# Kernel tuning notes

Hardware: AMD Instinct MI355X
Metric: run time of the kernel (lower is better)

## Reference

```python
import jax, jax.numpy as jnp
import numpy as np

B, S, IN_DIM, OUT_DIM, G = 8, 2048, 512, 256, 8
CHUNK = 128  # positions per scan step; per-chunk phi = CHUNK*O*O*G floats
EPS = 1e-5   # torch LayerNorm default


def make_periods():
    # periods[i,j,g] = i*(O*G) + j*G + g + 2
    i = jnp.arange(OUT_DIM, dtype=jnp.float32)[:, None, None]
    j = jnp.arange(OUT_DIM, dtype=jnp.float32)[None, :, None]
    g = jnp.arange(G, dtype=jnp.float32)[None, None, :]
    return i * (OUT_DIM * G) + j * G + g + 2.0


def setup_inputs() -> dict:
    key = jax.random.key(0)
    ks = jax.random.split(key, 4)
    x = jax.random.normal(ks[0], (B, S, IN_DIM), dtype=jnp.float32)
    positions = jnp.arange(S, dtype=jnp.int64 if jax.config.jax_enable_x64 else jnp.int32)
    M = jax.random.uniform(ks[1], (OUT_DIM, IN_DIM), minval=-0.5, maxval=0.5, dtype=jnp.float32)
    P = jax.random.uniform(ks[2], (OUT_DIM, OUT_DIM, G), minval=-0.1, maxval=0.1, dtype=jnp.float32)
    W_res = jax.random.uniform(ks[3], (OUT_DIM, IN_DIM), minval=-0.1, maxval=0.1, dtype=jnp.float32)
    ln_scale = jnp.ones((OUT_DIM,), dtype=jnp.float32)
    ln_bias = jnp.zeros((OUT_DIM,), dtype=jnp.float32)
    periods = make_periods()
    return {"x": x, "M": M, "P": P, "W_res": W_res, "ln_scale": ln_scale,
            "ln_bias": ln_bias, "periods": periods, "positions": positions}


def layer_norm(h, scale, bias):
    mu = jnp.mean(h, axis=-1, keepdims=True)
    var = jnp.mean(jnp.square(h - mu), axis=-1, keepdims=True)  # biased, like torch
    return (h - mu) * jax.lax.rsqrt(var + EPS) * scale + bias


def reference(x, M, P, W_res, ln_scale, ln_bias, periods, positions):
    # x: (B,S,in), M: (out,in), P: (out,out,G), periods: (out,out,G)
    x_trans = layer_norm(jnp.einsum('bsi,oi->bso', x, M), ln_scale, ln_bias)

    two_pi = jnp.float32(2.0 * np.pi)
    pos_chunks = positions.astype(jnp.float32).reshape(-1, CHUNK)  # (S/CHUNK, CHUNK)

    def body(carry, pos):
        # phi: (CHUNK, O, O, G); reduce over g first to avoid the huge 5D tensor
        phi = jnp.cos(two_pi * pos[:, None, None, None] / periods)
        A = jnp.einsum('sijg,ijg->sij', phi, P)  # (CHUNK, O, O)
        return carry, A

    _, A = jax.lax.scan(body, 0, pos_chunks)
    A = A.reshape(S, OUT_DIM, OUT_DIM)  # A[s,i,j] = sum_g P[i,j,g]*cos(2*pi*k_s/T_ijg)

    Nk = jnp.einsum('bsj,sij->bsi', x_trans, A)  # (B,S,out)
    residual = jnp.einsum('bsi,oi->bso', x, W_res)  # separate residual proj
    return Nk + residual
```

## Files before the change

kernel.cpp:

```cpp
#include <hip/hip_runtime.h>
#include <hip/hip_bf16.h>
#include <math.h>

#define B_   8
#define S_   2048
#define IN_  512
#define OUT_ 256
#define G_   8


typedef float  f32x2  __attribute__((ext_vector_type(2)));
typedef float  f32x4  __attribute__((ext_vector_type(4)));
typedef short  s16x8  __attribute__((ext_vector_type(8)));
typedef __bf16 bf16x8 __attribute__((ext_vector_type(8)));
typedef unsigned short u16x8 __attribute__((ext_vector_type(8)));

__device__ __forceinline__ float cos2pi(float f) {
#if __has_builtin(__builtin_amdgcn_cosf)
    return __builtin_amdgcn_cosf(f);
#else
    return __cosf(6.28318530717958647692f * f);
#endif
}

__device__ __forceinline__ float fractf_(float f) {
#if __has_builtin(__builtin_amdgcn_fractf)
    return __builtin_amdgcn_fractf(f);
#else
    return f - floorf(f);
#endif
}

__device__ __forceinline__ unsigned short f2bf(float f) {
    unsigned u = __builtin_bit_cast(unsigned, f);
    u += 0x7fffu + ((u >> 16) & 1u);
    return (unsigned short)(u >> 16);
}

template <typename T>
__device__ __forceinline__ auto atomF_(T* p, T v, int) -> decltype(unsafeAtomicAdd(p, v)) {
    return unsafeAtomicAdd(p, v);
}
template <typename T>
__device__ __forceinline__ T atomF_(T* p, T v, long) {
    return atomicAdd(p, v);
}
__device__ __forceinline__ void atomAddF(float* p, float v) { atomF_(p, v, 0); }

template <typename T>
__device__ __forceinline__ auto mfma_bf16_(T a, T b, f32x4 c, int)
    -> decltype(__builtin_amdgcn_mfma_f32_16x16x32_bf16(a, b, c, 0, 0, 0)) {
    return __builtin_amdgcn_mfma_f32_16x16x32_bf16(a, b, c, 0, 0, 0);
}
template <typename T>
__device__ __forceinline__ auto mfma_bf16_(T a, T b, f32x4 c, long)
    -> decltype(__builtin_amdgcn_mfma_f32_16x16x32_bf16(__builtin_bit_cast(bf16x8, a),
                                                        __builtin_bit_cast(bf16x8, b), c, 0, 0, 0)) {
    return __builtin_amdgcn_mfma_f32_16x16x32_bf16(__builtin_bit_cast(bf16x8, a),
                                                   __builtin_bit_cast(bf16x8, b), c, 0, 0, 0);
}
__device__ __forceinline__ f32x4 mfma_bf16(s16x8 a, s16x8 b, f32x4 c) {
    return mfma_bf16_(a, b, c, 0);
}

__device__ __forceinline__ void gld16(const void* g, void* l) {
    __builtin_amdgcn_global_load_lds((const __attribute__((address_space(1))) unsigned int*)g,
                                     (__attribute__((address_space(3))) unsigned int*)l,
                                     16, 0, 0);
}

__device__ __forceinline__ f32x2 lo2(float4 v) { f32x2 r; r.x = v.x; r.y = v.y; return r; }
__device__ __forceinline__ f32x2 hi2(float4 v) { f32x2 r; r.x = v.z; r.y = v.w; return r; }

__device__ __forceinline__ void prep_one(const float* __restrict__ P,
                                         const float* __restrict__ periods,
                                         float4* __restrict__ PTK, int tid) {
    const int j = tid >> 8, i = tid & 255;
    float p[8], iT[8], k2[8];
#pragma unroll
    for (int g = 0; g < 8; ++g) {
        const int idx = (i * 256 + j) * 8 + g;
        p[g]  = P[idx];
        iT[g] = 1.0f / periods[idx];
        k2[g] = 2.0f * cos2pi(iT[g]);
    }
    float4* base = PTK + (size_t)(j * 6) * 256 + i;
    base[0]    = make_float4(p[0],  p[1],  p[2],  p[3]);
    base[256]  = make_float4(p[4],  p[5],  p[6],  p[7]);
    base[512]  = make_float4(iT[0], iT[1], iT[2], iT[3]);
    base[768]  = make_float4(iT[4], iT[5], iT[6], iT[7]);
    base[1024] = make_float4(k2[0], k2[1], k2[2], k2[3]);
    base[1280] = make_float4(k2[4], k2[5], k2[6], k2[7]);
}

__global__ __launch_bounds__(256) void cvt_prep(const float* __restrict__ x,
                                                const float* __restrict__ M,
                                                const float* __restrict__ Wres,
                                                const float* __restrict__ P,
                                                const float* __restrict__ periods,
                                                unsigned short* __restrict__ Xb,
                                                unsigned short* __restrict__ Wb,
                                                float4* __restrict__ PTK) {
    const int bid = blockIdx.x;
    if (bid >= 4224) {
        prep_one(P, periods, PTK, (bid - 4224) * 256 + threadIdx.x);
        return;
    }
    const float* src;
    unsigned short* dst;
    if (bid < 4096) {
        const int idx = bid * 256 + threadIdx.x;
        src = x + (size_t)idx * 8;
        dst = Xb + (size_t)idx * 8;
    } else {
        const int idx = (bid - 4096) * 256 + threadIdx.x;
        const int row = idx >> 6;
        const int col = (idx & 63) * 8;
        src = (row < 256) ? (M + (size_t)row * 512 + col)
                          : (Wres + (size_t)(row - 256) * 512 + col);
        dst = Wb + (size_t)row * 512 + col;
    }
    const float4 v0 = *(const float4*)(src);
    const float4 v1 = *(const float4*)(src + 4);
    u16x8 o;
    o[0] = f2bf(v0.x); o[1] = f2bf(v0.y); o[2] = f2bf(v0.z); o[3] = f2bf(v0.w);
    o[4] = f2bf(v1.x); o[5] = f2bf(v1.y); o[6] = f2bf(v1.z); o[7] = f2bf(v1.w);
    *(u16x8*)dst = o;
}

__global__ __launch_bounds__(256) void cvt_xw(const float* __restrict__ x,
                                              const float* __restrict__ M,
                                              const float* __restrict__ Wres,
                                              unsigned short* __restrict__ Xb,
                                              unsigned short* __restrict__ Wb) {
    const int bid = blockIdx.x;
    const float* src;
    unsigned short* dst;
    if (bid < 4096) {
        const int idx = bid * 256 + threadIdx.x;
        src = x + (size_t)idx * 8;
        dst = Xb + (size_t)idx * 8;
    } else {
        const int idx = (bid - 4096) * 256 + threadIdx.x;
        const int row = idx >> 6;
        const int col = (idx & 63) * 8;
        src = (row < 256) ? (M + (size_t)row * 512 + col)
                          : (Wres + (size_t)(row - 256) * 512 + col);
        dst = Wb + (size_t)row * 512 + col;
    }
    const float4 v0 = *(const float4*)(src);
    const float4 v1 = *(const float4*)(src + 4);
    u16x8 o;
    o[0] = f2bf(v0.x); o[1] = f2bf(v0.y); o[2] = f2bf(v0.z); o[3] = f2bf(v0.w);
    o[4] = f2bf(v1.x); o[5] = f2bf(v1.y); o[6] = f2bf(v1.z); o[7] = f2bf(v1.w);
    *(u16x8*)dst = o;
}

__global__ __launch_bounds__(256) void prep_ptk(const float* __restrict__ P,
                                                const float* __restrict__ periods,
                                                float4* __restrict__ PTK) {
    prep_one(P, periods, PTK, blockIdx.x * 256 + threadIdx.x);
}

__global__ __launch_bounds__(256) void gemm_mfma(const unsigned short* __restrict__ Xb,
                                                 const unsigned short* __restrict__ Wb,
                                                 float* __restrict__ y,
                                                 float* __restrict__ out) {
    __shared__ __align__(16) unsigned short At[64 * 64];
    __shared__ __align__(16) unsigned short Bt[128 * 64];
    const int t    = threadIdx.x;
    const int col0 = blockIdx.x * 128;
    const int row0 = blockIdx.y * 64;

    const unsigned short* ga[2]; int la[2];
    const unsigned short* gb[4]; int lb[4];
#pragma unroll
    for (int cc = 0; cc < 2; ++cc) {
        const int L = cc * 256 + t;
        const int r = L >> 3;
        const int c = (L & 7) ^ (r & 7);
        ga[cc] = Xb + (size_t)(row0 + r) * 512 + c * 8;
        la[cc] = L * 8;
    }
#pragma unroll
    for (int cc = 0; cc < 4; ++cc) {
        const int L = cc * 256 + t;
        const int r = L >> 3;
        const int c = (L & 7) ^ (r & 7);
        gb[cc] = Wb + (size_t)(col0 + r) * 512 + c * 8;
        lb[cc] = L * 8;
    }

    const int lane = t & 63;
    const int wave = t >> 6;
    const int wn   = wave * 32;
    const int quad = lane >> 4;
    const int l16  = lane & 15;

    f32x4 acc[4][2];
#pragma unroll
    for (int mi = 0; mi < 4; ++mi)
#pragma unroll
        for (int ni = 0; ni < 2; ++ni) acc[mi][ni] = {0.0f, 0.0f, 0.0f, 0.0f};

    for (int k0 = 0; k0 < 512; k0 += 64) {
        __syncthreads();
#pragma unroll
        for (int cc = 0; cc < 2; ++cc) gld16(ga[cc] + k0, At + la[cc]);
#pragma unroll
        for (int cc = 0; cc < 4; ++cc) gld16(gb[cc] + k0, Bt + lb[cc]);
        __syncthreads();
#pragma unroll
        for (int ks = 0; ks < 2; ++ks) {
            const int cc = (ks * 4 + quad) ^ (l16 & 7);
            s16x8 af[4], bf[2];
#pragma unroll
            for (int mi = 0; mi < 4; ++mi) {
                const int ra = mi * 16 + l16;
                af[mi] = *(const s16x8*)(At + (ra * 8 + cc) * 8);
            }
#pragma unroll
            for (int ni = 0; ni < 2; ++ni) {
                const int rb = wn + ni * 16 + l16;
                bf[ni] = *(const s16x8*)(Bt + (rb * 8 + cc) * 8);
            }
#pragma unroll
            for (int mi = 0; mi < 4; ++mi)
#pragma unroll
                for (int ni = 0; ni < 2; ++ni)
                    acc[mi][ni] = mfma_bf16(af[mi], bf[ni], acc[mi][ni]);
        }
    }

    float* dst   = (col0 < 256) ? y : out;
    const int cb = (col0 & 255) + wn;
#pragma unroll
    for (int mi = 0; mi < 4; ++mi) {
        const int rbase = row0 + mi * 16 + quad * 4;
#pragma unroll
        for (int ni = 0; ni < 2; ++ni) {
            const int col = cb + ni * 16 + l16;
#pragma unroll
            for (int rg = 0; rg < 4; ++rg)
                dst[(size_t)(rbase + rg) * 256 + col] = acc[mi][ni][rg];
        }
    }
}

__global__ __launch_bounds__(256) void gemm_kernel(const float* __restrict__ x,
                                                   const float* __restrict__ M,
                                                   const float* __restrict__ Wres,
                                                   float* __restrict__ y,
                                                   float* __restrict__ out) {
    __shared__ float As[8][132];
    __shared__ float Bs[8][132];
    const int ct = blockIdx.x;
    const int rt = blockIdx.y;
    const int t  = threadIdx.x;
    const int row0 = rt * 128;
    const float* W = (ct < 2) ? M : Wres;
    const int wcol0 = (ct & 1) * 128;
    float acc[8][8];
#pragma unroll
    for (int r = 0; r < 8; ++r)
#pragma unroll
        for (int c = 0; c < 8; ++c) acc[r][c] = 0.0f;
    const int lr = t >> 1;
    const int lk = (t & 1) << 2;
    for (int k0 = 0; k0 < 512; k0 += 8) {
        float4 av = *(const float4*)(x + (size_t)(row0 + lr) * 512 + k0 + lk);
        float4 bv = *(const float4*)(W + (size_t)(wcol0 + lr) * 512 + k0 + lk);
        __syncthreads();
        As[lk + 0][lr] = av.x; As[lk + 1][lr] = av.y; As[lk + 2][lr] = av.z; As[lk + 3][lr] = av.w;
        Bs[lk + 0][lr] = bv.x; Bs[lk + 1][lr] = bv.y; Bs[lk + 2][lr] = bv.z; Bs[lk + 3][lr] = bv.w;
        __syncthreads();
        const int tx = t & 15, ty = t >> 4;
#pragma unroll
        for (int kk = 0; kk < 8; ++kk) {
            const float4 a0 = *(const float4*)&As[kk][ty * 8];
            const float4 a1 = *(const float4*)&As[kk][ty * 8 + 4];
            const float4 b0 = *(const float4*)&Bs[kk][tx * 8];
            const float4 b1 = *(const float4*)&Bs[kk][tx * 8 + 4];
            const float ar[8] = {a0.x, a0.y, a0.z, a0.w, a1.x, a1.y, a1.z, a1.w};
            const float br[8] = {b0.x, b0.y, b0.z, b0.w, b1.x, b1.y, b1.z, b1.w};
#pragma unroll
            for (int r = 0; r < 8; ++r)
#pragma unroll
                for (int c = 0; c < 8; ++c) acc[r][c] = fmaf(ar[r], br[c], acc[r][c]);
        }
    }
    const int tx = t & 15, ty = t >> 4;
    float* dst = (ct < 2) ? y : out;
    const int cbase = (ct & 1) * 128 + tx * 8;
#pragma unroll
    for (int r = 0; r < 8; ++r) {
        float4 v0 = {acc[r][0], acc[r][1], acc[r][2], acc[r][3]};
        float4 v1 = {acc[r][4], acc[r][5], acc[r][6], acc[r][7]};
        float* p = dst + (size_t)(row0 + ty * 8 + r) * 256 + cbase;
        *(float4*)(p)     = v0;
        *(float4*)(p + 4) = v1;
    }
}

__global__ __launch_bounds__(256) void ln_kernel(float* __restrict__ y,
                                                 const float* __restrict__ scale,
                                                 const float* __restrict__ bias) {
    const int t    = threadIdx.x;
    const int row  = blockIdx.x * 4 + (t >> 6);
    const int lane = t & 63;
    float* p = y + (size_t)row * 256 + lane * 4;
    float4 v = *(float4*)p;
    float s  = v.x + v.y + v.z + v.w;
    float ss = v.x * v.x + v.y * v.y + v.z * v.z + v.w * v.w;
#pragma unroll
    for (int off = 32; off > 0; off >>= 1) {
        s  += __shfl_xor(s, off);
        ss += __shfl_xor(ss, off);
    }
    const float mu  = s * (1.0f / 256.0f);
    const float var = ss * (1.0f / 256.0f) - mu * mu;
    const float rs  = rsqrtf(var + 1e-5f);
    float4 sc = *(const float4*)(scale + lane * 4);
    float4 bi = *(const float4*)(bias + lane * 4);
    float4 o;
    o.x = (v.x - mu) * rs * sc.x + bi.x;
    o.y = (v.y - mu) * rs * sc.y + bi.y;
    o.z = (v.z - mu) * rs * sc.z + bi.z;
    o.w = (v.w - mu) * rs * sc.w + bi.w;
    *(float4*)p = o;
}

__global__ __launch_bounds__(256, 4) void cosnk_pk(const float4* __restrict__ PTK,
                                                   const float* __restrict__ xt,
                                                   float* __restrict__ out) {
    __shared__ float xs[128 * 64];
    const int t  = threadIdx.x;
    const int bx = blockIdx.x;
    const int ih = (bx >> 2) & 1;
    const int rid = ((bx >> 3) << 2) | (bx & 3);
    const int stile = rid >> 1;
    const int jh = rid & 1;
    const int s0 = stile * 8;
    const int jbase = jh * 128;

    {
        const int slot = t >> 2;
        const int st   = slot >> 3;
        const int b    = slot & 7;
        const int jg   = t & 3;
        const float* src = xt + (size_t)(b * S_ + s0 + st) * 256 + jbase + jg * 32;
#pragma unroll
        for (int q = 0; q < 8; ++q) {
            float4 v = *(const float4*)(src + 4 * q);
            const int jl = jg * 32 + 4 * q;
            xs[(jl + 0) * 64 + slot] = v.x;
            xs[(jl + 1) * 64 + slot] = v.y;
            xs[(jl + 2) * 64 + slot] = v.z;
            xs[(jl + 3) * 64 + slot] = v.w;
        }
    }
    __syncthreads();

    const int i   = ih * 128 + (t & 127);
    const int jq  = t >> 7;
    const int jl0 = jq * 64;
    const float sv0 = (float)s0;
    f32x2 sv0v; sv0v.x = sv0; sv0v.y = sv0;

    f32x2 accP[8][4];
#pragma unroll
    for (int s = 0; s < 8; ++s)
#pragma unroll
        for (int q = 0; q < 4; ++q) { accP[s][q].x = 0.0f; accP[s][q].y = 0.0f; }

    const float4* ptk = PTK + (size_t)(jbase + jl0) * 1536 + i;
    float4 qp0 = ptk[0],    qp1 = ptk[256];
    float4 qt0 = ptk[512],  qt1 = ptk[768];
    float4 qk0 = ptk[1024], qk1 = ptk[1280];

#define CHEBP(p2_, t2_, k2_)                                \
    do {                                                    \
        f32x2 f0 = sv0v * (t2_);                            \
        f0.x = fractf_(f0.x); f0.y = fractf_(f0.y);         \
        f32x2 c0; c0.x = cos2pi(f0.x); c0.y = cos2pi(f0.y); \
        f32x2 f1 = f0 + (t2_);                              \
        f1.x = fractf_(f1.x); f1.y = fractf_(f1.y);         \
        f32x2 c1; c1.x = cos2pi(f1.x); c1.y = cos2pi(f1.y); \
        f32x2 c2 = (k2_) * c1 - c0;                         \
        f32x2 c3 = (k2_) * c2 - c1;                         \
        f32x2 c4 = (k2_) * c3 - c2;                         \
        f32x2 c5 = (k2_) * c4 - c3;                         \
        f32x2 c6 = (k2_) * c5 - c4;                         \
        f32x2 c7 = (k2_) * c6 - c5;                         \
        A0 += (p2_) * c0; A1 += (p2_) * c1;                 \
        A2 += (p2_) * c2; A3 += (p2_) * c3;                 \
        A4 += (p2_) * c4; A5 += (p2_) * c5;                 \
        A6 += (p2_) * c6; A7 += (p2_) * c7;                 \
    } while (0)

    for (int jj = 0; jj < 64; ++jj) {
        const float4* pn = ptk + ((jj < 63) ? 1536 : 0);
        const float4 n0 = pn[0],   n1 = pn[256],  n2 = pn[512];
        const float4 n3 = pn[768], n4 = pn[1024], n5 = pn[1280];

        f32x2 A0 = {0.f, 0.f}, A1 = {0.f, 0.f}, A2 = {0.f, 0.f}, A3 = {0.f, 0.f};
        f32x2 A4 = {0.f, 0.f}, A5 = {0.f, 0.f}, A6 = {0.f, 0.f}, A7 = {0.f, 0.f};
        CHEBP(lo2(qp0), lo2(qt0), lo2(qk0));
        CHEBP(hi2(qp0), hi2(qt0), hi2(qk0));
        CHEBP(lo2(qp1), lo2(qt1), lo2(qk1));
        CHEBP(hi2(qp1), hi2(qt1), hi2(qk1));

        const float as_[8] = {A0.x + A0.y, A1.x + A1.y, A2.x + A2.y, A3.x + A3.y,
                              A4.x + A4.y, A5.x + A5.y, A6.x + A6.y, A7.x + A7.y};

        const float* xrow = &xs[(jl0 + jj) * 64];
#pragma unroll
        for (int s = 0; s < 8; ++s) {
            const float4 xa = *(const float4*)(xrow + s * 8);
            const float4 xb = *(const float4*)(xrow + s * 8 + 4);
            f32x2 av; av.x = as_[s]; av.y = as_[s];
            accP[s][0] += av * lo2(xa);
            accP[s][1] += av * hi2(xa);
            accP[s][2] += av * lo2(xb);
            accP[s][3] += av * hi2(xb);
        }
        qp0 = n0; qp1 = n1; qt0 = n2; qt1 = n3; qk0 = n4; qk1 = n5;
        ptk = pn;
    }
#undef CHEBP

    __syncthreads();
    const int tl = t & 127;
    if (jq) {
#pragma unroll
        for (int slot = 0; slot < 64; ++slot) {
            const int st = slot >> 3, b = slot & 7;
            xs[slot * 128 + tl] = accP[st][b >> 1][b & 1];
        }
    }
    __syncthreads();
    if (!jq) {
#pragma unroll
        for (int slot = 0; slot < 64; ++slot) {
            const int st = slot >> 3, b = slot & 7;
            const float v = accP[st][b >> 1][b & 1] + xs[slot * 128 + tl];
            atomAddF(&out[(size_t)(b * S_ + s0 + st) * 256 + i], v);
        }
    }
}

extern "C" void kernel_launch(void* const* d_in, const int* in_sizes, int n_in,
                              void* d_out, int out_size, void* d_ws, size_t ws_size,
                              hipStream_t stream) {
    const float* x        = (const float*)d_in[0];
    const float* M        = (const float*)d_in[1];
    const float* P        = (const float*)d_in[2];
    const float* Wres     = (const float*)d_in[3];
    const float* ln_scale = (const float*)d_in[4];
    const float* ln_bias  = (const float*)d_in[5];
    const float* periods  = (const float*)d_in[6];

    float* out = (float*)d_out;
    char*  wsb = (char*)d_ws;
    const size_t MB = 1024 * 1024;
    float* y = (float*)wsb;
    unsigned short* Xb = (unsigned short*)(wsb + 16 * MB);
    unsigned short* Wb = (unsigned short*)(wsb + 32 * MB);

    const bool big  = (ws_size >= 39 * MB);
    const bool mfma = (ws_size >= (size_t)34078720);

    float4* PTK;
    if (big) {
        PTK = (float4*)(wsb + 33 * MB);
        cvt_prep<<<4480, 256, 0, stream>>>(x, M, Wres, P, periods, Xb, Wb, PTK);
        dim3 ggrid(4, 256);
        gemm_mfma<<<ggrid, 256, 0, stream>>>(Xb, Wb, y, out);
    } else if (mfma) {
        PTK = (float4*)(wsb + 16 * MB);
        cvt_xw<<<4224, 256, 0, stream>>>(x, M, Wres, Xb, Wb);
        dim3 ggrid(4, 256);
        gemm_mfma<<<ggrid, 256, 0, stream>>>(Xb, Wb, y, out);
        prep_ptk<<<256, 256, 0, stream>>>(P, periods, PTK);
    } else {
        PTK = (float4*)(wsb + 16 * MB);
        dim3 ggrid(4, 128);
        gemm_kernel<<<ggrid, 256, 0, stream>>>(x, M, Wres, y, out);
        prep_ptk<<<256, 256, 0, stream>>>(P, periods, PTK);
    }

    ln_kernel<<<4096, 256, 0, stream>>>(y, ln_scale, ln_bias);

    cosnk_pk<<<1024, 256, 0, stream>>>(PTK, y, out);
}
```

Measured before the change: 234.4 us.

## Use fp16 dot2 for cos-weighted accumulation and shrink GEMM column tiles

```diff
diff --git a/kernel.cpp b/kernel.cpp
--- a/kernel.cpp
+++ b/kernel.cpp
@@ -9,11 +9,13 @@
 #define G_   8
 
 
-typedef float  f32x2  __attribute__((ext_vector_type(2)));
-typedef float  f32x4  __attribute__((ext_vector_type(4)));
-typedef short  s16x8  __attribute__((ext_vector_type(8)));
-typedef __bf16 bf16x8 __attribute__((ext_vector_type(8)));
+typedef float    f32x2  __attribute__((ext_vector_type(2)));
+typedef float    f32x4  __attribute__((ext_vector_type(4)));
+typedef short    s16x8  __attribute__((ext_vector_type(8)));
+typedef __bf16   bf16x8 __attribute__((ext_vector_type(8)));
 typedef unsigned short u16x8 __attribute__((ext_vector_type(8)));
+typedef _Float16 h2     __attribute__((ext_vector_type(2)));
+typedef _Float16 h16x8  __attribute__((ext_vector_type(8)));
 
 __device__ __forceinline__ float cos2pi(float f) {
 #if __has_builtin(__builtin_amdgcn_cosf)
@@ -36,6 +38,37 @@
     u += 0x7fffu + ((u >> 16) & 1u);
     return (unsigned short)(u >> 16);
 }
+
+__device__ __forceinline__ h2 pkrtz2(float a, float b) {
+#if __has_builtin(__builtin_amdgcn_cvt_pkrtz)
+    return __builtin_bit_cast(h2, __builtin_amdgcn_cvt_pkrtz(a, b));
+#else
+    h2 r; r[0] = (_Float16)a; r[1] = (_Float16)b; return r;
+#endif
+}
+
+#if __has_builtin(__builtin_amdgcn_fdot2)
+template <typename T>
+__device__ __forceinline__ auto fdot2_impl(T a, T b, float c, int)
+    -> decltype(__builtin_amdgcn_fdot2(a, b, c, false)) {
+    return __builtin_amdgcn_fdot2(a, b, c, false);
+}
+typedef __fp16 fp16v2 __attribute__((ext_vector_type(2)));
+template <typename T>
+__device__ __forceinline__ auto fdot2_impl(T a, T b, float c, long)
+    -> decltype(__builtin_amdgcn_fdot2(__builtin_bit_cast(fp16v2, a),
+                                       __builtin_bit_cast(fp16v2, b), c, false)) {
+    return __builtin_amdgcn_fdot2(__builtin_bit_cast(fp16v2, a),
+                                  __builtin_bit_cast(fp16v2, b), c, false);
+}
+__device__ __forceinline__ float fdot2_(h2 a, h2 b, float c) {
+    return fdot2_impl(a, b, c, 0);
+}
+#else
+__device__ __forceinline__ float fdot2_(h2 a, h2 b, float c) {
+    return c + (float)a[0] * (float)b[0] + (float)a[1] * (float)b[1];
+}
+#endif
 
 template <typename T>
 __device__ __forceinline__ auto atomF_(T* p, T v, int) -> decltype(unsafeAtomicAdd(p, v)) {
@@ -167,68 +200,58 @@
                                                  float* __restrict__ y,
                                                  float* __restrict__ out) {
     __shared__ __align__(16) unsigned short At[64 * 64];
-    __shared__ __align__(16) unsigned short Bt[128 * 64];
+    __shared__ __align__(16) unsigned short Bt[64 * 64];
     const int t    = threadIdx.x;
-    const int col0 = blockIdx.x * 128;
+    const int col0 = blockIdx.x * 64;
     const int row0 = blockIdx.y * 64;
 
     const unsigned short* ga[2]; int la[2];
-    const unsigned short* gb[4]; int lb[4];
+    const unsigned short* gb[2]; int lb[2];
 #pragma unroll
     for (int cc = 0; cc < 2; ++cc) {
         const int L = cc * 256 + t;
         const int r = L >> 3;
         const int c = (L & 7) ^ (r & 7);
         ga[cc] = Xb + (size_t)(row0 + r) * 512 + c * 8;
+        gb[cc] = Wb + (size_t)(col0 + r) * 512 + c * 8;
         la[cc] = L * 8;
-    }
-#pragma unroll
-    for (int cc = 0; cc < 4; ++cc) {
-        const int L = cc * 256 + t;
-        const int r = L >> 3;
-        const int c = (L & 7) ^ (r & 7);
-        gb[cc] = Wb + (size_t)(col0 + r) * 512 + c * 8;
         lb[cc] = L * 8;
     }
 
     const int lane = t & 63;
     const int wave = t >> 6;
-    const int wn   = wave * 32;
+    const int wn   = wave * 16;
     const int quad = lane >> 4;
     const int l16  = lane & 15;
 
-    f32x4 acc[4][2];
-#pragma unroll
-    for (int mi = 0; mi < 4; ++mi)
-#pragma unroll
-        for (int ni = 0; ni < 2; ++ni) acc[mi][ni] = {0.0f, 0.0f, 0.0f, 0.0f};
+    f32x4 acc[4];
+#pragma unroll
+    for (int mi = 0; mi < 4; ++mi) acc[mi] = {0.0f, 0.0f, 0.0f, 0.0f};
 
     for (int k0 = 0; k0 < 512; k0 += 64) {
         __syncthreads();
 #pragma unroll
-        for (int cc = 0; cc < 2; ++cc) gld16(ga[cc] + k0, At + la[cc]);
-#pragma unroll
-        for (int cc = 0; cc < 4; ++cc) gld16(gb[cc] + k0, Bt + lb[cc]);
+        for (int cc = 0; cc < 2; ++cc) {
+            gld16(ga[cc] + k0, At + la[cc]);
+            gld16(gb[cc] + k0, Bt + lb[cc]);
+        }
         __syncthreads();
 #pragma unroll
         for (int ks = 0; ks < 2; ++ks) {
             const int cc = (ks * 4 + quad) ^ (l16 & 7);
-            s16x8 af[4], bf[2];
+            s16x8 af[4], bf;
 #pragma unroll
             for (int mi = 0; mi < 4; ++mi) {
                 const int ra = mi * 16 + l16;
                 af[mi] = *(const s16x8*)(At + (ra * 8 + cc) * 8);
             }
-#pragma unroll
-            for (int ni = 0; ni < 2; ++ni) {
-                const int rb = wn + ni * 16 + l16;
-                bf[ni] = *(const s16x8*)(Bt + (rb * 8 + cc) * 8);
+            {
+                const int rb = wn + l16;
+                bf = *(const s16x8*)(Bt + (rb * 8 + cc) * 8);
             }
 #pragma unroll
             for (int mi = 0; mi < 4; ++mi)
-#pragma unroll
-                for (int ni = 0; ni < 2; ++ni)
-                    acc[mi][ni] = mfma_bf16(af[mi], bf[ni], acc[mi][ni]);
+                acc[mi] = mfma_bf16(af[mi], bf, acc[mi]);
         }
     }
 
@@ -237,13 +260,10 @@
 #pragma unroll
     for (int mi = 0; mi < 4; ++mi) {
         const int rbase = row0 + mi * 16 + quad * 4;
-#pragma unroll
-        for (int ni = 0; ni < 2; ++ni) {
-            const int col = cb + ni * 16 + l16;
-#pragma unroll
-            for (int rg = 0; rg < 4; ++rg)
-                dst[(size_t)(rbase + rg) * 256 + col] = acc[mi][ni][rg];
-        }
+        const int col = cb + l16;
+#pragma unroll
+        for (int rg = 0; rg < 4; ++rg)
+            dst[(size_t)(rbase + rg) * 256 + col] = acc[mi][rg];
     }
 }
 
@@ -330,10 +350,13 @@
     *(float4*)p = o;
 }
 
-__global__ __launch_bounds__(256, 4) void cosnk_pk(const float4* __restrict__ PTK,
+__global__ __launch_bounds__(256, 4) void cosnk_fd(const float4* __restrict__ PTK,
                                                    const float* __restrict__ xt,
                                                    float* __restrict__ out) {
-    __shared__ float xs[128 * 64];
+    __shared__ __align__(16) char smem[32768];
+    h2*    xsh = (h2*)smem;
+    float* red = (float*)smem;
+
     const int t  = threadIdx.x;
     const int bx = blockIdx.x;
     const int ih = (bx >> 2) & 1;
@@ -352,11 +375,9 @@
 #pragma unroll
         for (int q = 0; q < 8; ++q) {
             float4 v = *(const float4*)(src + 4 * q);
-            const int jl = jg * 32 + 4 * q;
-            xs[(jl + 0) * 64 + slot] = v.x;
-            xs[(jl + 1) * 64 + slot] = v.y;
-            xs[(jl + 2) * 64 + slot] = v.z;
-            xs[(jl + 3) * 64 + slot] = v.w;
+            const int jp = jg * 16 + 2 * q;
+            xsh[(jp + 0) * 64 + slot] = pkrtz2(v.x, v.y);
+            xsh[(jp + 1) * 64 + slot] = pkrtz2(v.z, v.w);
         }
     }
     __syncthreads();
@@ -367,16 +388,18 @@
     const float sv0 = (float)s0;
     f32x2 sv0v; sv0v.x = sv0; sv0v.y = sv0;
 
-    f32x2 accP[8][4];
+    float acc[8][8];
 #pragma unroll
     for (int s = 0; s < 8; ++s)
 #pragma unroll
-        for (int q = 0; q < 4; ++q) { accP[s][q].x = 0.0f; accP[s][q].y = 0.0f; }
+        for (int b = 0; b < 8; ++b) acc[s][b] = 0.0f;
 
     const float4* ptk = PTK + (size_t)(jbase + jl0) * 1536 + i;
     float4 qp0 = ptk[0],    qp1 = ptk[256];
     float4 qt0 = ptk[512],  qt1 = ptk[768];
     float4 qk0 = ptk[1024], qk1 = ptk[1280];
+
+    float asv[8];
 
 #define CHEBP(p2_, t2_, k2_)                                \
     do {                                                    \
@@ -398,6 +421,7 @@
         A6 += (p2_) * c6; A7 += (p2_) * c7;                 \
     } while (0)
 
+#pragma unroll 2
     for (int jj = 0; jj < 64; ++jj) {
         const float4* pn = ptk + ((jj < 63) ? 1536 : 0);
         const float4 n0 = pn[0],   n1 = pn[256],  n2 = pn[512];
@@ -413,16 +437,25 @@
         const float as_[8] = {A0.x + A0.y, A1.x + A1.y, A2.x + A2.y, A3.x + A3.y,
                               A4.x + A4.y, A5.x + A5.y, A6.x + A6.y, A7.x + A7.y};
 
-        const float* xrow = &xs[(jl0 + jj) * 64];
-#pragma unroll
-        for (int s = 0; s < 8; ++s) {
-            const float4 xa = *(const float4*)(xrow + s * 8);
-            const float4 xb = *(const float4*)(xrow + s * 8 + 4);
-            f32x2 av; av.x = as_[s]; av.y = as_[s];
-            accP[s][0] += av * lo2(xa);
-            accP[s][1] += av * hi2(xa);
-            accP[s][2] += av * lo2(xb);
-            accP[s][3] += av * hi2(xb);
+        if ((jj & 1) == 0) {
+#pragma unroll
+            for (int s = 0; s < 8; ++s) asv[s] = as_[s];
+        } else {
+            const h2* xrow = xsh + (size_t)(jq * 32 + (jj >> 1)) * 64;
+#pragma unroll
+            for (int s = 0; s < 8; ++s) {
+                const h2 ap = pkrtz2(asv[s], as_[s]);
+                const h16x8 hx0 = *(const h16x8*)(xrow + s * 8);
+                const h16x8 hx1 = *(const h16x8*)(xrow + s * 8 + 4);
+                acc[s][0] = fdot2_(ap, __builtin_shufflevector(hx0, hx0, 0, 1), acc[s][0]);
+                acc[s][1] = fdot2_(ap, __builtin_shufflevector(hx0, hx0, 2, 3), acc[s][1]);
+                acc[s][2] = fdot2_(ap, __builtin_shufflevector(hx0, hx0, 4, 5), acc[s][2]);
+                acc[s][3] = fdot2_(ap, __builtin_shufflevector(hx0, hx0, 6, 7), acc[s][3]);
+                acc[s][4] = fdot2_(ap, __builtin_shufflevector(hx1, hx1, 0, 1), acc[s][4]);
+                acc[s][5] = fdot2_(ap, __builtin_shufflevector(hx1, hx1, 2, 3), acc[s][5]);
+                acc[s][6] = fdot2_(ap, __builtin_shufflevector(hx1, hx1, 4, 5), acc[s][6]);
+                acc[s][7] = fdot2_(ap, __builtin_shufflevector(hx1, hx1, 6, 7), acc[s][7]);
+            }
         }
         qp0 = n0; qp1 = n1; qt0 = n2; qt1 = n3; qk0 = n4; qk1 = n5;
         ptk = pn;
@@ -433,17 +466,15 @@
     const int tl = t & 127;
     if (jq) {
 #pragma unroll
+        for (int slot = 0; slot < 64; ++slot)
+            red[slot * 128 + tl] = acc[slot >> 3][slot & 7];
+    }
+    __syncthreads();
+    if (!jq) {
+#pragma unroll
         for (int slot = 0; slot < 64; ++slot) {
             const int st = slot >> 3, b = slot & 7;
-            xs[slot * 128 + tl] = accP[st][b >> 1][b & 1];
-        }
-    }
-    __syncthreads();
-    if (!jq) {
-#pragma unroll
-        for (int slot = 0; slot < 64; ++slot) {
-            const int st = slot >> 3, b = slot & 7;
-            const float v = accP[st][b >> 1][b & 1] + xs[slot * 128 + tl];
+            const float v = acc[st][b] + red[slot * 128 + tl];
             atomAddF(&out[(size_t)(b * S_ + s0 + st) * 256 + i], v);
         }
     }
@@ -474,12 +505,12 @@
     if (big) {
         PTK = (float4*)(wsb + 33 * MB);
         cvt_prep<<<4480, 256, 0, stream>>>(x, M, Wres, P, periods, Xb, Wb, PTK);
-        dim3 ggrid(4, 256);
+        dim3 ggrid(8, 256);
         gemm_mfma<<<ggrid, 256, 0, stream>>>(Xb, Wb, y, out);
     } else if (mfma) {
         PTK = (float4*)(wsb + 16 * MB);
         cvt_xw<<<4224, 256, 0, stream>>>(x, M, Wres, Xb, Wb);
-        dim3 ggrid(4, 256);
+        dim3 ggrid(8, 256);
         gemm_mfma<<<ggrid, 256, 0, stream>>>(Xb, Wb, y, out);
         prep_ptk<<<256, 256, 0, stream>>>(P, periods, PTK);
     } else {
@@ -491,5 +522,5 @@
 
     ln_kernel<<<4096, 256, 0, stream>>>(y, ln_scale, ln_bias);
 
-    cosnk_pk<<<1024, 256, 0, stream>>>(PTK, y, out);
-}
+    cosnk_fd<<<1024, 256, 0, stream>>>(PTK, y, out);
+}
```

Result: slower. 240.8 us (+2.7%).
